# Kernel tuning notes

Measured on AMD Instinct MI355X. Metric: run time of the kernel, lower is better.

## Reference

```python
import jax, jax.numpy as jnp
import numpy as np
from jax import lax

B, DIM, H, W = 8, 256, 48, 48
HEADS, DH = 8, 32
K, S = 5, 2
P = K // 2
SCALE = DH ** -0.5
EPS = 1e-5


def setup_inputs() -> dict:
    key = jax.random.key(0)
    ks = jax.random.split(key, 12)
    w = lambda k, sh: jax.random.normal(k, sh, jnp.float32) * 0.02
    return {
        'x': jax.random.normal(ks[0], (B, DIM, H, W), jnp.float32),
        'kv': jax.random.normal(ks[1], (B, DIM, H, W), jnp.float32),
        'wq': w(ks[2], (DIM, DIM)), 'bq': jnp.zeros((DIM,), jnp.float32),
        'wk': w(ks[3], (DIM, DIM)), 'bk': jnp.zeros((DIM,), jnp.float32),
        'wv': w(ks[4], (DIM, DIM)), 'bv': jnp.zeros((DIM,), jnp.float32),
        'w_dw': w(ks[5], (DH, 1, K, K)), 'b_dw': jnp.zeros((DH,), jnp.float32),
        'ln_w': jnp.ones((DH,), jnp.float32), 'ln_b': jnp.zeros((DH,), jnp.float32),
        'w_off': w(ks[6], (2, DH)),
        'wo': w(ks[7], (DIM, DIM)), 'bo': jnp.zeros((DIM,), jnp.float32),
    }


def conv1x1(x, w, b=None):
    # x: (B, Cin, H, W), w: (Cout, Cin)
    y = jnp.einsum('oc,bchw->bohw', w, x)
    return y if b is None else y + b[None, :, None, None]


def grid_sample_bilinear(inp, grid):
    # inp: (N, C, Hh, Ww); grid: (N, Hg, Wg, 2) in (x, y), align_corners=True
    N, C, Hh, Ww = inp.shape
    gx = (grid[..., 0] + 1.0) * 0.5 * (Ww - 1)
    gy = (grid[..., 1] + 1.0) * 0.5 * (Hh - 1)
    x0 = jnp.floor(gx)
    y0 = jnp.floor(gy)
    wx = gx - x0  # frac weights for x1/y1 corners
    wy = gy - y0
    x0i = jnp.clip(x0.astype(jnp.int32), 0, Ww - 1)
    x1i = jnp.clip(x0.astype(jnp.int32) + 1, 0, Ww - 1)
    y0i = jnp.clip(y0.astype(jnp.int32), 0, Hh - 1)
    y1i = jnp.clip(y0.astype(jnp.int32) + 1, 0, Hh - 1)
    flat = inp.reshape(N, C, Hh * Ww)
    n = grid.shape[1] * grid.shape[2]

    def gather(yi, xi):
        idx = (yi * Ww + xi).reshape(N, 1, n)
        return jnp.take_along_axis(flat, jnp.broadcast_to(idx, (N, C, n)), axis=2)

    w00 = ((1 - wx) * (1 - wy)).reshape(N, 1, n)
    w01 = (wx * (1 - wy)).reshape(N, 1, n)
    w10 = ((1 - wx) * wy).reshape(N, 1, n)
    w11 = (wx * wy).reshape(N, 1, n)
    return (w00 * gather(y0i, x0i) + w01 * gather(y0i, x1i)
            + w10 * gather(y1i, x0i) + w11 * gather(y1i, x1i))  # (N, C, n)


def reference(x, kv, wq, bq, wk, bk, wv, bv, w_dw, b_dw, ln_w, ln_b, w_off, wo, bo):
    q = conv1x1(x, wq, bq)                      # (B, DIM, H, W)
    q_off = q.reshape(B * HEADS, DH, H, W)      # per-head channels
    # depthwise offset conv
    t = lax.conv_general_dilated(q_off, w_dw, (S, S), [(P, P), (P, P)],
                                 feature_group_count=DH,
                                 dimension_numbers=('NCHW', 'OIHW', 'NCHW'))
    t = t + b_dw[None, :, None, None]
    Hk, Wk = t.shape[2], t.shape[3]
    n = Hk * Wk
    # LayerNormProxy: LN over channel dim
    t = t.transpose(0, 2, 3, 1)                 # (BH, Hk, Wk, DH)
    mu = t.mean(-1, keepdims=True)
    var = ((t - mu) ** 2).mean(-1, keepdims=True)
    t = (t - mu) / jnp.sqrt(var + EPS) * ln_w + ln_b
    t = jax.nn.gelu(t, approximate=False)
    offset = jnp.einsum('oc,bhwc->bhwo', w_off, t)  # (BH, Hk, Wk, 2) as (y, x)
    # reference points, normalized to [-1, 1]
    ref_y = (jnp.linspace(0.5, Hk - 0.5, Hk, dtype=jnp.float32) / (Hk - 1.0)) * 2.0 - 1.0
    ref_x = (jnp.linspace(0.5, Wk - 0.5, Wk, dtype=jnp.float32) / (Wk - 1.0)) * 2.0 - 1.0
    ref = jnp.stack(jnp.meshgrid(ref_y, ref_x, indexing='ij'), axis=-1)  # (Hk, Wk, 2)
    pos = jnp.clip(offset + ref[None], -1.0, 1.0)
    grid = pos[..., ::-1]                       # (x, y) order for sampling
    kvs = grid_sample_bilinear(kv.reshape(B * HEADS, DH, H, W), grid)  # (BH, DH, n)
    kv4 = kvs.reshape(B, DIM, 1, n)
    k = conv1x1(kv4, wk, bk).reshape(B * HEADS, DH, n)
    v = conv1x1(kv4, wv, bv).reshape(B * HEADS, DH, n)
    qf = q.reshape(B * HEADS, DH, H * W)
    attn = jax.nn.softmax(jnp.einsum('bcm,bcn->bmn', qf, k) * SCALE, axis=2)
    out = jnp.einsum('bmn,bcn->bcm', attn, v).reshape(B, DIM, H, W)
    return conv1x1(out, wo, bo)
```

## Files before the change

### kernel.cpp

```cpp
#include <hip/hip_runtime.h>
#include <hip/hip_bf16.h>
#include <cstddef>

#define BB 8
#define DIM 256
#define HH 48
#define WW 48
#define HW 2304
#define HEADS 8
#define DH 32
#define BH 64
#define HK 24
#define WK 24
#define NN 576
#define SCALE 0.17677669529663687f
#define EPSF 1e-5f

typedef __attribute__((ext_vector_type(8))) short short8;
typedef __attribute__((ext_vector_type(4))) float f32x4;

static __device__ inline short f2bf_s(float f) {
  __hip_bfloat16 h = __float2bfloat16(f);
  return *reinterpret_cast<short*>(&h);
}

template <typename T> __device__ inline T cvt_out(float v);
template <> __device__ inline float cvt_out<float>(float v) { return v; }
template <> __device__ inline __hip_bfloat16 cvt_out<__hip_bfloat16>(float v) {
  return __float2bfloat16(v);
}

static __device__ inline unsigned pkrnd(float a, float b) {
  unsigned ua = __builtin_bit_cast(unsigned, a) + 0x8000u;
  unsigned ub = __builtin_bit_cast(unsigned, b) + 0x8000u;
  return __builtin_amdgcn_perm(ub, ua, 0x07060302);
}

static __device__ inline void split8(const float* xf, short8& bh, short8& bl) {
  union { unsigned u[4]; short8 v; } H, L;
#pragma unroll
  for (int p = 0; p < 4; p++) {
    float x0 = xf[2 * p], x1 = xf[2 * p + 1];
    unsigned u0 = __builtin_bit_cast(unsigned, x0) & 0xffff0000u;
    unsigned u1 = __builtin_bit_cast(unsigned, x1) & 0xffff0000u;
    float l0 = x0 - __builtin_bit_cast(float, u0);
    float l1 = x1 - __builtin_bit_cast(float, u1);
    H.u[p] = __builtin_amdgcn_perm(u1, u0, 0x07060302);
    L.u[p] = __builtin_amdgcn_perm(__builtin_bit_cast(unsigned, l1),
                                   __builtin_bit_cast(unsigned, l0), 0x07060302);
  }
  bh = H.v;
  bl = L.v;
}

__global__ __launch_bounds__(256) void split4(
    const float* __restrict__ w0, const float* __restrict__ w1,
    const float* __restrict__ w2, const float* __restrict__ w3,
    short* __restrict__ h0, short* __restrict__ l0,
    short* __restrict__ h1, short* __restrict__ l1,
    short* __restrict__ h2, short* __restrict__ l2,
    short* __restrict__ h3, short* __restrict__ l3) {
  const float* srcs[4] = {w0, w1, w2, w3};
  short* his[4] = {h0, h1, h2, h3};
  short* los[4] = {l0, l1, l2, l3};
  int sel = blockIdx.x >> 8;
  int i = (blockIdx.x & 255) * 256 + threadIdx.x;
  float v = srcs[sel][i];
  unsigned u = __builtin_bit_cast(unsigned, v) & 0xffff0000u;
  float rem = v - __builtin_bit_cast(float, u);
  his[sel][i] = (short)(u >> 16);
  los[sel][i] = (short)(__builtin_bit_cast(unsigned, rem) >> 16);
}

template <typename OT>
__global__ __launch_bounds__(64) void gemm_axf_mfma(const short* __restrict__ Wh,
                                                    const short* __restrict__ Wl,
                                                    const float* __restrict__ bias,
                                                    const float* __restrict__ X,
                                                    OT* __restrict__ Y, int M) {
  const int lane = threadIdx.x;
  const int quad = lane >> 4, l15 = lane & 15;
  const int b = blockIdx.z;
  const int oBase = blockIdx.y * 32;
  const int mBase = blockIdx.x * 64;
  const float* Xq = X + ((size_t)b * 256 + quad * 8) * M;

  f32x4 acc[2][4] = {};
  for (int kc = 0; kc < 256; kc += 32) {
    short8 ah0 = *(const short8*)(Wh + (size_t)(oBase + l15) * 256 + kc + quad * 8);
    short8 al0 = *(const short8*)(Wl + (size_t)(oBase + l15) * 256 + kc + quad * 8);
    short8 ah1 = *(const short8*)(Wh + (size_t)(oBase + 16 + l15) * 256 + kc + quad * 8);
    short8 al1 = *(const short8*)(Wl + (size_t)(oBase + 16 + l15) * 256 + kc + quad * 8);
#pragma unroll
    for (int mt = 0; mt < 4; mt++) {
      float xf[8];
      const float* xp = Xq + (size_t)kc * M + mBase + mt * 16 + l15;
#pragma unroll
      for (int j = 0; j < 8; j++) xf[j] = xp[(size_t)j * M];
      short8 bh, bl;
      split8(xf, bh, bl);
      acc[0][mt] = __builtin_amdgcn_mfma_f32_16x16x32_bf16(ah0, bh, acc[0][mt], 0, 0, 0);
      acc[0][mt] = __builtin_amdgcn_mfma_f32_16x16x32_bf16(al0, bh, acc[0][mt], 0, 0, 0);
      acc[0][mt] = __builtin_amdgcn_mfma_f32_16x16x32_bf16(ah0, bl, acc[0][mt], 0, 0, 0);
      acc[1][mt] = __builtin_amdgcn_mfma_f32_16x16x32_bf16(ah1, bh, acc[1][mt], 0, 0, 0);
      acc[1][mt] = __builtin_amdgcn_mfma_f32_16x16x32_bf16(al1, bh, acc[1][mt], 0, 0, 0);
      acc[1][mt] = __builtin_amdgcn_mfma_f32_16x16x32_bf16(ah1, bl, acc[1][mt], 0, 0, 0);
    }
  }

#pragma unroll
  for (int os = 0; os < 2; os++)
#pragma unroll
    for (int r = 0; r < 4; r++) {
      int o = oBase + os * 16 + quad * 4 + r;
      float bs = bias[o];
      OT* yp = Y + ((size_t)b * 256 + o) * M + mBase + l15;
#pragma unroll
      for (int mt = 0; mt < 4; mt++) yp[mt * 16] = cvt_out<OT>(acc[os][mt][r] + bs);
    }
}

__global__ __launch_bounds__(64) void k_gemm_mfma(const short* __restrict__ Wh,
                                                  const short* __restrict__ Wl,
                                                  const float* __restrict__ bias,
                                                  const float* __restrict__ X,
                                                  short* __restrict__ Y) {
  const int lane = threadIdx.x;
  const int quad = lane >> 4, l15 = lane & 15;
  const int b = blockIdx.z;
  const int nBase = blockIdx.x * 32;
  const int oBase = blockIdx.y * 64;
  const float* Xq = X + ((size_t)b * 256 + quad * 8) * NN;

  f32x4 acc[2][4] = {};
  for (int kc = 0; kc < 256; kc += 32) {
    short8 ah[2], al[2];
#pragma unroll
    for (int ns = 0; ns < 2; ns++) {
      float xf[8];
      const float* xp = Xq + (size_t)kc * NN + nBase + ns * 16 + l15;
#pragma unroll
      for (int j = 0; j < 8; j++) xf[j] = xp[(size_t)j * NN];
      split8(xf, ah[ns], al[ns]);
    }
#pragma unroll
    for (int ot = 0; ot < 4; ot++) {
      short8 bh = *(const short8*)(Wh + (size_t)(oBase + ot * 16 + l15) * 256 + kc + quad * 8);
      short8 bl = *(const short8*)(Wl + (size_t)(oBase + ot * 16 + l15) * 256 + kc + quad * 8);
#pragma unroll
      for (int ns = 0; ns < 2; ns++) {
        acc[ns][ot] = __builtin_amdgcn_mfma_f32_16x16x32_bf16(ah[ns], bh, acc[ns][ot], 0, 0, 0);
        acc[ns][ot] = __builtin_amdgcn_mfma_f32_16x16x32_bf16(al[ns], bh, acc[ns][ot], 0, 0, 0);
        acc[ns][ot] = __builtin_amdgcn_mfma_f32_16x16x32_bf16(ah[ns], bl, acc[ns][ot], 0, 0, 0);
      }
    }
  }

  float bs[4];
#pragma unroll
  for (int ot = 0; ot < 4; ot++) bs[ot] = bias[oBase + ot * 16 + l15];
#pragma unroll
  for (int ns = 0; ns < 2; ns++)
#pragma unroll
    for (int r = 0; r < 4; r++) {
      int n = nBase + ns * 16 + quad * 4 + r;
      short* yp = Y + ((size_t)b * NN + n) * 256 + oBase + l15;
#pragma unroll
      for (int ot = 0; ot < 4; ot++) yp[ot * 16] = f2bf_s(acc[ns][ot][r] + bs[ot]);
    }
}

__global__ __launch_bounds__(64) void dw_sample_kernel(
    const float* __restrict__ q, const float* __restrict__ kv,
    const float* __restrict__ w_dw, const float* __restrict__ b_dw,
    const float* __restrict__ ln_w, const float* __restrict__ ln_b,
    const float* __restrict__ w_off, float* __restrict__ kvs) {
  __shared__ float s_wdw[DH * 25];
  __shared__ float s_bdw[DH], s_lnw[DH], s_lnb[DH], s_woff[2 * DH];
  const int tid = threadIdx.x;
  for (int i = tid; i < DH * 25; i += 64) s_wdw[i] = w_dw[i];
  if (tid < DH) { s_bdw[tid] = b_dw[tid]; s_lnw[tid] = ln_w[tid]; s_lnb[tid] = ln_b[tid]; }
  if (tid < 2 * DH) s_woff[tid] = w_off[tid];
  __syncthreads();

  const int gid = blockIdx.x * 64 + tid;
  const int bh = gid / NN;
  const int n = gid - bh * NN;
  const int yk = n / WK, xk = n - yk * WK;

  const float* qb = q + (size_t)bh * DH * HW;
  float t[DH];
#pragma unroll
  for (int c = 0; c < DH; c++) t[c] = s_bdw[c];

  const int y0r = yk * 2 - 2, x0r = xk * 2 - 2;
  for (int dy = 0; dy < 5; dy++) {
    int y = y0r + dy;
    if (y < 0 || y >= HH) continue;
    for (int dx = 0; dx < 5; dx++) {
      int x = x0r + dx;
      if (x < 0 || x >= WW) continue;
      int off = y * WW + x;
      int widx = dy * 5 + dx;
#pragma unroll
      for (int c = 0; c < DH; c++)
        t[c] += s_wdw[c * 25 + widx] * qb[c * HW + off];
    }
  }

  float mu = 0.f;
#pragma unroll
  for (int c = 0; c < DH; c++) mu += t[c];
  mu *= (1.0f / DH);
  float var = 0.f;
#pragma unroll
  for (int c = 0; c < DH; c++) { float d = t[c] - mu; var += d * d; }
  var *= (1.0f / DH);
  float rstd = rsqrtf(var + EPSF);

  float o0 = 0.f, o1 = 0.f;
#pragma unroll
  for (int c = 0; c < DH; c++) {
    float xn = (t[c] - mu) * rstd * s_lnw[c] + s_lnb[c];
    float g = 0.5f * xn * (1.0f + erff(xn * 0.70710678118654752f));
    o0 += s_woff[c] * g;
    o1 += s_woff[DH + c] * g;
  }

  const float ref_y = (0.5f + (float)yk) / 23.0f * 2.0f - 1.0f;
  const float ref_x = (0.5f + (float)xk) / 23.0f * 2.0f - 1.0f;
  float py = fminf(fmaxf(o0 + ref_y, -1.0f), 1.0f);
  float px = fminf(fmaxf(o1 + ref_x, -1.0f), 1.0f);

  float gx = (px + 1.0f) * 0.5f * 47.0f;
  float gy = (py + 1.0f) * 0.5f * 47.0f;
  float x0f = floorf(gx), y0f = floorf(gy);
  float wx = gx - x0f, wy = gy - y0f;
  int x0 = (int)x0f, y0 = (int)y0f;
  int x0i = min(max(x0, 0), WW - 1);
  int x1i = min(max(x0 + 1, 0), WW - 1);
  int y0i = min(max(y0, 0), HH - 1);
  int y1i = min(max(y0 + 1, 0), HH - 1);
  float w00 = (1.f - wx) * (1.f - wy);
  float w01 = wx * (1.f - wy);
  float w10 = (1.f - wx) * wy;
  float w11 = wx * wy;
  int i00 = y0i * WW + x0i, i01 = y0i * WW + x1i;
  int i10 = y1i * WW + x0i, i11 = y1i * WW + x1i;

  const float* kvb = kv + (size_t)bh * DH * HW;
#pragma unroll
  for (int c = 0; c < DH; c++) {
    const float* p = kvb + (size_t)c * HW;
    float val = w00 * p[i00] + w01 * p[i01] + w10 * p[i10] + w11 * p[i11];
    kvs[((size_t)bh * DH + c) * NN + n] = val;
  }
}

__global__ __launch_bounds__(256) void attn_mfma(const float* __restrict__ q,
                                                 const short* __restrict__ Kb,
                                                 const short* __restrict__ Vb,
                                                 short* __restrict__ O) {
  __shared__ int smem[2][4][2][256];
  const int tid = threadIdx.x;
  const int wave = tid >> 6;
  const int lane = tid & 63;
  const int quad = lane >> 4;
  const int l15 = lane & 15;
  const int bh = blockIdx.y;
  const int b = bh >> 3, head = bh & 7;
  const int mBase = blockIdx.x * 128 + wave * 32;

  short8 bq[2];
#pragma unroll
  for (int mt = 0; mt < 2; mt++) {
    const float* qp = q + ((size_t)bh * DH + quad * 8) * HW + mBase + mt * 16 + l15;
    short8 v;
#pragma unroll
    for (int j = 0; j < 8; j++) v[j] = f2bf_s(qp[(size_t)j * HW] * SCALE);
    bq[mt] = v;
  }

  const short* kbase = Kb + (size_t)b * NN * 256 + head * DH + quad * 8;
  const short* vb0 = Vb + ((size_t)b * 256 + head * DH + l15) * NN + quad * 8;
  const short* vb1 = vb0 + (size_t)16 * NN;

  f32x4 oacc[2][2] = {};
  float dsum[2] = {0.f, 0.f};

  const int row16 = l15 * 16;
  const int wr0 = row16 + (((quad >> 1) ^ (l15 & 3)) << 2) + ((quad & 1) << 1);
  const int wr1 = row16 + (((2 + (quad >> 1)) ^ (l15 & 3)) << 2) + ((quad & 1) << 1);
  const int rd = row16 + ((quad ^ (l15 & 3)) << 2);

  short8 ka0 = *(const short8*)(kbase + (size_t)l15 * 256);
  short8 ka1 = *(const short8*)(kbase + (size_t)(16 + l15) * 256);

  for (int it = 0; it < NN / 32; it++) {
    const int nb = it * 32;
    short8 va0 = *(const short8*)(vb0 + nb);
    short8 va1 = *(const short8*)(vb1 + nb);
    f32x4 z = {0.f, 0.f, 0.f, 0.f};
    f32x4 st[2][2];
    st[0][0] = __builtin_amdgcn_mfma_f32_16x16x32_bf16(ka0, bq[0], z, 0, 0, 0);
    st[0][1] = __builtin_amdgcn_mfma_f32_16x16x32_bf16(ka1, bq[0], z, 0, 0, 0);
    st[1][0] = __builtin_amdgcn_mfma_f32_16x16x32_bf16(ka0, bq[1], z, 0, 0, 0);
    st[1][1] = __builtin_amdgcn_mfma_f32_16x16x32_bf16(ka1, bq[1], z, 0, 0, 0);
    if (it + 1 < NN / 32) {
      ka0 = *(const short8*)(kbase + (size_t)(nb + 32 + l15) * 256);
      ka1 = *(const short8*)(kbase + (size_t)(nb + 48 + l15) * 256);
    }
    int* sm = &smem[it & 1][wave][0][0];
#pragma unroll
    for (int mt = 0; mt < 2; mt++) {
      float p0 = __expf(st[mt][0][0]), p1 = __expf(st[mt][0][1]);
      float p2 = __expf(st[mt][0][2]), p3 = __expf(st[mt][0][3]);
      float p4 = __expf(st[mt][1][0]), p5 = __expf(st[mt][1][1]);
      float p6 = __expf(st[mt][1][2]), p7 = __expf(st[mt][1][3]);
      dsum[mt] += ((p0 + p1) + (p2 + p3)) + ((p4 + p5) + (p6 + p7));
      int* base = sm + mt * 256;
      *(int2*)(base + wr0) = make_int2((int)pkrnd(p0, p1), (int)pkrnd(p2, p3));
      *(int2*)(base + wr1) = make_int2((int)pkrnd(p4, p5), (int)pkrnd(p6, p7));
    }
#pragma unroll
    for (int mt = 0; mt < 2; mt++) {
      short8 pa = *(short8*)(sm + mt * 256 + rd);
      oacc[mt][0] = __builtin_amdgcn_mfma_f32_16x16x32_bf16(pa, va0, oacc[mt][0], 0, 0, 0);
      oacc[mt][1] = __builtin_amdgcn_mfma_f32_16x16x32_bf16(pa, va1, oacc[mt][1], 0, 0, 0);
    }
  }

#pragma unroll
  for (int mt = 0; mt < 2; mt++) {
    float d = dsum[mt];
    d += __shfl_xor(d, 16);
    d += __shfl_xor(d, 32);
    short* ob = O + ((size_t)b * HW + mBase + mt * 16) * 256 + head * DH + l15;
#pragma unroll
    for (int r = 0; r < 4; r++) {
      float dr = __shfl(d, quad * 4 + r);
      float inv = 1.0f / dr;
      ob[(size_t)(quad * 4 + r) * 256] = f2bf_s(oacc[mt][0][r] * inv);
      ob[(size_t)(quad * 4 + r) * 256 + 16] = f2bf_s(oacc[mt][1][r] * inv);
    }
  }
}

__global__ __launch_bounds__(256) void wo_gemm_mfma(const short* __restrict__ Whi,
                                                    const short* __restrict__ Wlo,
                                                    const float* __restrict__ bias,
                                                    const short* __restrict__ X,
                                                    float* __restrict__ Y) {
  const int tid = threadIdx.x;
  const int wave = tid >> 6;
  const int lane = tid & 63;
  const int quad = lane >> 4;
  const int l15 = lane & 15;
  const int b = blockIdx.z;
  const int oBase = blockIdx.y * 64 + wave * 16;
  const int mBase = blockIdx.x * 64;

  const short* wh = Whi + (size_t)(oBase + l15) * 256 + quad * 8;
  const short* wl = Wlo + (size_t)(oBase + l15) * 256 + quad * 8;
  const short* xb = X + ((size_t)b * HW + mBase) * 256 + quad * 8;

  f32x4 acc[4] = {};

  for (int k = 0; k < 256; k += 32) {
    short8 ah = *(const short8*)(wh + k);
    short8 al = *(const short8*)(wl + k);
#pragma unroll
    for (int mt = 0; mt < 4; mt++) {
      short8 bx = *(const short8*)(xb + (size_t)(mt * 16 + l15) * 256 + k);
      acc[mt] = __builtin_amdgcn_mfma_f32_16x16x32_bf16(ah, bx, acc[mt], 0, 0, 0);
      acc[mt] = __builtin_amdgcn_mfma_f32_16x16x32_bf16(al, bx, acc[mt], 0, 0, 0);
    }
  }

#pragma unroll
  for (int r = 0; r < 4; r++) {
    int o = oBase + quad * 4 + r;
    float bs = bias[o];
    float* yrow = Y + ((size_t)b * 256 + o) * HW + mBase + l15;
#pragma unroll
    for (int mt = 0; mt < 4; mt++) {
      yrow[mt * 16] = acc[mt][r] + bs;
    }
  }
}

extern "C" void kernel_launch(void* const* d_in, const int* in_sizes, int n_in,
                              void* d_out, int out_size, void* d_ws, size_t ws_size,
                              hipStream_t stream) {
  const float* x    = (const float*)d_in[0];
  const float* kv   = (const float*)d_in[1];
  const float* wq   = (const float*)d_in[2];
  const float* bq   = (const float*)d_in[3];
  const float* wk   = (const float*)d_in[4];
  const float* bk   = (const float*)d_in[5];
  const float* wv   = (const float*)d_in[6];
  const float* bv   = (const float*)d_in[7];
  const float* w_dw = (const float*)d_in[8];
  const float* b_dw = (const float*)d_in[9];
  const float* ln_w = (const float*)d_in[10];
  const float* ln_b = (const float*)d_in[11];
  const float* w_off= (const float*)d_in[12];
  const float* wo   = (const float*)d_in[13];
  const float* bo   = (const float*)d_in[14];
  float* out = (float*)d_out;
  float* ws = (float*)d_ws;

  float* q   = ws;
  float* kvs = ws + 4718592;
  short* O   = (short*)(ws + 4718592);
  short* Kb  = (short*)(ws + 7077888);
  short* Vb  = (short*)(ws + 7667712);
  short* Wqh = (short*)(ws + 8257536);
  short* Wql = Wqh + 65536;
  short* Wkh = Wql + 65536;
  short* Wkl = Wkh + 65536;
  short* Wvh = Wkl + 65536;
  short* Wvl = Wvh + 65536;
  short* Woh = Wvl + 65536;
  short* Wol = Woh + 65536;

  split4<<<dim3(1024), dim3(256), 0, stream>>>(wq, wk, wv, wo, Wqh, Wql, Wkh, Wkl,
                                               Wvh, Wvl, Woh, Wol);
  gemm_axf_mfma<float><<<dim3(HW / 64, 8, BB), dim3(64), 0, stream>>>(
      Wqh, Wql, bq, x, q, HW);
  dw_sample_kernel<<<dim3(BH * NN / 64), dim3(64), 0, stream>>>(
      q, kv, w_dw, b_dw, ln_w, ln_b, w_off, kvs);
  k_gemm_mfma<<<dim3(NN / 32, 4, BB), dim3(64), 0, stream>>>(Wkh, Wkl, bk, kvs, Kb);
  gemm_axf_mfma<__hip_bfloat16><<<dim3(NN / 64, 8, BB), dim3(64), 0, stream>>>(
      Wvh, Wvl, bv, kvs, (__hip_bfloat16*)Vb, NN);
  attn_mfma<<<dim3(HW / 128, BH), dim3(256), 0, stream>>>(q, Kb, Vb, O);
  wo_gemm_mfma<<<dim3(HW / 64, 4, BB), dim3(256), 0, stream>>>(Woh, Wol, bo, O, out);
}
```

Measured before the change: 270.8 us.

## Retile Q projection, split dw_sample channels across lanes, shrink attention per-wave tile

Adds a dedicated Q-projection GEMM kernel in which each 256-thread block computes all 256 output channels for a 64-pixel tile, so every X load is reused across four output slices. The depthwise/offset/sample kernel now spreads the 32 channels of one sample across four lane groups of 8, using shuffles for the LayerNorm and offset reductions, which gives 4x more threads and smaller register arrays. The attention kernel processes 16 query rows per wave instead of 32, doubling the grid to raise parallelism, at the cost of reloading K/V per wave more often. The LDS swizzle pattern is also changed.

```diff
diff --git a/kernel.cpp b/kernel.cpp
--- a/kernel.cpp
+++ b/kernel.cpp
@@ -72,6 +72,57 @@
   los[sel][i] = (short)(__builtin_bit_cast(unsigned, rem) >> 16);
 }
 
+__global__ __launch_bounds__(256) void gemm_q_mfma(const short* __restrict__ Wh,
+                                                   const short* __restrict__ Wl,
+                                                   const float* __restrict__ bias,
+                                                   const float* __restrict__ X,
+                                                   float* __restrict__ Y) {
+  const int tid = threadIdx.x;
+  const int wave = tid >> 6;
+  const int lane = tid & 63;
+  const int quad = lane >> 4, l15 = lane & 15;
+  const int b = blockIdx.y;
+  const int oBase = wave * 64;
+  const int mBase = blockIdx.x * 64;
+  const float* Xq = X + ((size_t)b * 256 + quad * 8) * HW;
+
+  f32x4 acc[4][4] = {};
+  for (int kc = 0; kc < 256; kc += 32) {
+    short8 ah[4], al[4];
+#pragma unroll
+    for (int os = 0; os < 4; os++) {
+      ah[os] = *(const short8*)(Wh + (size_t)(oBase + os * 16 + l15) * 256 + kc + quad * 8);
+      al[os] = *(const short8*)(Wl + (size_t)(oBase + os * 16 + l15) * 256 + kc + quad * 8);
+    }
+#pragma unroll
+    for (int mt = 0; mt < 4; mt++) {
+      float xf[8];
+      const float* xp = Xq + (size_t)kc * HW + mBase + mt * 16 + l15;
+#pragma unroll
+      for (int j = 0; j < 8; j++) xf[j] = xp[(size_t)j * HW];
+      short8 bh, bl;
+      split8(xf, bh, bl);
+#pragma unroll
+      for (int os = 0; os < 4; os++) {
+        acc[os][mt] = __builtin_amdgcn_mfma_f32_16x16x32_bf16(ah[os], bh, acc[os][mt], 0, 0, 0);
+        acc[os][mt] = __builtin_amdgcn_mfma_f32_16x16x32_bf16(al[os], bh, acc[os][mt], 0, 0, 0);
+        acc[os][mt] = __builtin_amdgcn_mfma_f32_16x16x32_bf16(ah[os], bl, acc[os][mt], 0, 0, 0);
+      }
+    }
+  }
+
+#pragma unroll
+  for (int os = 0; os < 4; os++)
+#pragma unroll
+    for (int r = 0; r < 4; r++) {
+      int o = oBase + os * 16 + quad * 4 + r;
+      float bs = bias[o];
+      float* yp = Y + ((size_t)b * 256 + o) * HW + mBase + l15;
+#pragma unroll
+      for (int mt = 0; mt < 4; mt++) yp[mt * 16] = acc[os][mt][r] + bs;
+    }
+}
+
 template <typename OT>
 __global__ __launch_bounds__(64) void gemm_axf_mfma(const short* __restrict__ Wh,
                                                     const short* __restrict__ Wl,
@@ -183,15 +234,17 @@
   if (tid < 2 * DH) s_woff[tid] = w_off[tid];
   __syncthreads();
 
-  const int gid = blockIdx.x * 64 + tid;
-  const int bh = gid / NN;
-  const int n = gid - bh * NN;
+  const int nl = tid & 15, cg = tid >> 4;
+  const int c0 = cg * 8;
+  const int bh = blockIdx.x / (NN / 16);
+  const int ntile = blockIdx.x - bh * (NN / 16);
+  const int n = ntile * 16 + nl;
   const int yk = n / WK, xk = n - yk * WK;
 
   const float* qb = q + (size_t)bh * DH * HW;
-  float t[DH];
-#pragma unroll
-  for (int c = 0; c < DH; c++) t[c] = s_bdw[c];
+  float t[8];
+#pragma unroll
+  for (int j = 0; j < 8; j++) t[j] = s_bdw[c0 + j];
 
   const int y0r = yk * 2 - 2, x0r = xk * 2 - 2;
   for (int dy = 0; dy < 5; dy++) {
@@ -203,29 +256,37 @@
       int off = y * WW + x;
       int widx = dy * 5 + dx;
 #pragma unroll
-      for (int c = 0; c < DH; c++)
-        t[c] += s_wdw[c * 25 + widx] * qb[c * HW + off];
+      for (int j = 0; j < 8; j++)
+        t[j] += s_wdw[(c0 + j) * 25 + widx] * qb[(size_t)(c0 + j) * HW + off];
     }
   }
 
   float mu = 0.f;
 #pragma unroll
-  for (int c = 0; c < DH; c++) mu += t[c];
+  for (int j = 0; j < 8; j++) mu += t[j];
+  mu += __shfl_xor(mu, 16);
+  mu += __shfl_xor(mu, 32);
   mu *= (1.0f / DH);
   float var = 0.f;
 #pragma unroll
-  for (int c = 0; c < DH; c++) { float d = t[c] - mu; var += d * d; }
+  for (int j = 0; j < 8; j++) { float d = t[j] - mu; var += d * d; }
+  var += __shfl_xor(var, 16);
+  var += __shfl_xor(var, 32);
   var *= (1.0f / DH);
   float rstd = rsqrtf(var + EPSF);
 
   float o0 = 0.f, o1 = 0.f;
 #pragma unroll
-  for (int c = 0; c < DH; c++) {
-    float xn = (t[c] - mu) * rstd * s_lnw[c] + s_lnb[c];
+  for (int j = 0; j < 8; j++) {
+    float xn = (t[j] - mu) * rstd * s_lnw[c0 + j] + s_lnb[c0 + j];
     float g = 0.5f * xn * (1.0f + erff(xn * 0.70710678118654752f));
-    o0 += s_woff[c] * g;
-    o1 += s_woff[DH + c] * g;
-  }
+    o0 += s_woff[c0 + j] * g;
+    o1 += s_woff[DH + c0 + j] * g;
+  }
+  o0 += __shfl_xor(o0, 16);
+  o0 += __shfl_xor(o0, 32);
+  o1 += __shfl_xor(o1, 16);
+  o1 += __shfl_xor(o1, 32);
 
   const float ref_y = (0.5f + (float)yk) / 23.0f * 2.0f - 1.0f;
   const float ref_x = (0.5f + (float)xk) / 23.0f * 2.0f - 1.0f;
@@ -248,12 +309,12 @@
   int i00 = y0i * WW + x0i, i01 = y0i * WW + x1i;
   int i10 = y1i * WW + x0i, i11 = y1i * WW + x1i;
 
-  const float* kvb = kv + (size_t)bh * DH * HW;
-#pragma unroll
-  for (int c = 0; c < DH; c++) {
-    const float* p = kvb + (size_t)c * HW;
+  const float* kvb = kv + ((size_t)bh * DH + c0) * HW;
+#pragma unroll
+  for (int j = 0; j < 8; j++) {
+    const float* p = kvb + (size_t)j * HW;
     float val = w00 * p[i00] + w01 * p[i01] + w10 * p[i10] + w11 * p[i11];
-    kvs[((size_t)bh * DH + c) * NN + n] = val;
+    kvs[((size_t)bh * DH + c0 + j) * NN + n] = val;
   }
 }
 
@@ -261,7 +322,7 @@
                                                  const short* __restrict__ Kb,
                                                  const short* __restrict__ Vb,
                                                  short* __restrict__ O) {
-  __shared__ int smem[2][4][2][256];
+  __shared__ int smem[2][4][256];
   const int tid = threadIdx.x;
   const int wave = tid >> 6;
   const int lane = tid & 63;
@@ -269,29 +330,27 @@
   const int l15 = lane & 15;
   const int bh = blockIdx.y;
   const int b = bh >> 3, head = bh & 7;
-  const int mBase = blockIdx.x * 128 + wave * 32;
-
-  short8 bq[2];
-#pragma unroll
-  for (int mt = 0; mt < 2; mt++) {
-    const float* qp = q + ((size_t)bh * DH + quad * 8) * HW + mBase + mt * 16 + l15;
-    short8 v;
-#pragma unroll
-    for (int j = 0; j < 8; j++) v[j] = f2bf_s(qp[(size_t)j * HW] * SCALE);
-    bq[mt] = v;
+  const int mBase = blockIdx.x * 64 + wave * 16;
+
+  short8 bq;
+  {
+    const float* qp = q + ((size_t)bh * DH + quad * 8) * HW + mBase + l15;
+#pragma unroll
+    for (int j = 0; j < 8; j++) bq[j] = f2bf_s(qp[(size_t)j * HW] * SCALE);
   }
 
   const short* kbase = Kb + (size_t)b * NN * 256 + head * DH + quad * 8;
   const short* vb0 = Vb + ((size_t)b * 256 + head * DH + l15) * NN + quad * 8;
   const short* vb1 = vb0 + (size_t)16 * NN;
 
-  f32x4 oacc[2][2] = {};
-  float dsum[2] = {0.f, 0.f};
-
+  f32x4 oacc0 = {}, oacc1 = {};
+  float dsum = 0.f;
+
+  const int g = (l15 >> 1) & 3;
   const int row16 = l15 * 16;
-  const int wr0 = row16 + (((quad >> 1) ^ (l15 & 3)) << 2) + ((quad & 1) << 1);
-  const int wr1 = row16 + (((2 + (quad >> 1)) ^ (l15 & 3)) << 2) + ((quad & 1) << 1);
-  const int rd = row16 + ((quad ^ (l15 & 3)) << 2);
+  const int wr0 = row16 + ((((quad >> 1)) ^ g) << 2) + ((quad & 1) << 1);
+  const int wr1 = row16 + (((2 + (quad >> 1)) ^ g) << 2) + ((quad & 1) << 1);
+  const int rd = row16 + ((quad ^ g) << 2);
 
   short8 ka0 = *(const short8*)(kbase + (size_t)l15 * 256);
   short8 ka1 = *(const short8*)(kbase + (size_t)(16 + l15) * 256);
@@ -301,48 +360,36 @@
     short8 va0 = *(const short8*)(vb0 + nb);
     short8 va1 = *(const short8*)(vb1 + nb);
     f32x4 z = {0.f, 0.f, 0.f, 0.f};
-    f32x4 st[2][2];
-    st[0][0] = __builtin_amdgcn_mfma_f32_16x16x32_bf16(ka0, bq[0], z, 0, 0, 0);
-    st[0][1] = __builtin_amdgcn_mfma_f32_16x16x32_bf16(ka1, bq[0], z, 0, 0, 0);
-    st[1][0] = __builtin_amdgcn_mfma_f32_16x16x32_bf16(ka0, bq[1], z, 0, 0, 0);
-    st[1][1] = __builtin_amdgcn_mfma_f32_16x16x32_bf16(ka1, bq[1], z, 0, 0, 0);
+    f32x4 st0 = __builtin_amdgcn_mfma_f32_16x16x32_bf16(ka0, bq, z, 0, 0, 0);
+    f32x4 st1 = __builtin_amdgcn_mfma_f32_16x16x32_bf16(ka1, bq, z, 0, 0, 0);
     if (it + 1 < NN / 32) {
       ka0 = *(const short8*)(kbase + (size_t)(nb + 32 + l15) * 256);
       ka1 = *(const short8*)(kbase + (size_t)(nb + 48 + l15) * 256);
     }
-    int* sm = &smem[it & 1][wave][0][0];
-#pragma unroll
-    for (int mt = 0; mt < 2; mt++) {
-      float p0 = __expf(st[mt][0][0]), p1 = __expf(st[mt][0][1]);
-      float p2 = __expf(st[mt][0][2]), p3 = __expf(st[mt][0][3]);
-      float p4 = __expf(st[mt][1][0]), p5 = __expf(st[mt][1][1]);
-      float p6 = __expf(st[mt][1][2]), p7 = __expf(st[mt][1][3]);
-      dsum[mt] += ((p0 + p1) + (p2 + p3)) + ((p4 + p5) + (p6 + p7));
-      int* base = sm + mt * 256;
-      *(int2*)(base + wr0) = make_int2((int)pkrnd(p0, p1), (int)pkrnd(p2, p3));
-      *(int2*)(base + wr1) = make_int2((int)pkrnd(p4, p5), (int)pkrnd(p6, p7));
-    }
-#pragma unroll
-    for (int mt = 0; mt < 2; mt++) {
-      short8 pa = *(short8*)(sm + mt * 256 + rd);
-      oacc[mt][0] = __builtin_amdgcn_mfma_f32_16x16x32_bf16(pa, va0, oacc[mt][0], 0, 0, 0);
-      oacc[mt][1] = __builtin_amdgcn_mfma_f32_16x16x32_bf16(pa, va1, oacc[mt][1], 0, 0, 0);
-    }
-  }
-
-#pragma unroll
-  for (int mt = 0; mt < 2; mt++) {
-    float d = dsum[mt];
-    d += __shfl_xor(d, 16);
-    d += __shfl_xor(d, 32);
-    short* ob = O + ((size_t)b * HW + mBase + mt * 16) * 256 + head * DH + l15;
-#pragma unroll
-    for (int r = 0; r < 4; r++) {
-      float dr = __shfl(d, quad * 4 + r);
-      float inv = 1.0f / dr;
-      ob[(size_t)(quad * 4 + r) * 256] = f2bf_s(oacc[mt][0][r] * inv);
-      ob[(size_t)(quad * 4 + r) * 256 + 16] = f2bf_s(oacc[mt][1][r] * inv);
-    }
+    float p0 = __expf(st0[0]), p1 = __expf(st0[1]);
+    float p2 = __expf(st0[2]), p3 = __expf(st0[3]);
+    float p4 = __expf(st1[0]), p5 = __expf(st1[1]);
+    float p6 = __expf(st1[2]), p7 = __expf(st1[3]);
+    dsum += ((p0 + p1) + (p2 + p3)) + ((p4 + p5) + (p6 + p7));
+    int* sm = &smem[it & 1][wave][0];
+    *(int2*)(sm + wr0) = make_int2((int)pkrnd(p0, p1), (int)pkrnd(p2, p3));
+    *(int2*)(sm + wr1) = make_int2((int)pkrnd(p4, p5), (int)pkrnd(p6, p7));
+    short8 pa = *(short8*)(sm + rd);
+    oacc0 = __builtin_amdgcn_mfma_f32_16x16x32_bf16(pa, va0, oacc0, 0, 0, 0);
+    oacc1 = __builtin_amdgcn_mfma_f32_16x16x32_bf16(pa, va1, oacc1, 0, 0, 0);
+  }
+
+  float d = dsum;
+  d += __shfl_xor(d, 16);
+  d += __shfl_xor(d, 32);
+
+  short* ob = O + ((size_t)b * HW + mBase) * 256 + head * DH + l15;
+#pragma unroll
+  for (int r = 0; r < 4; r++) {
+    float dr = __shfl(d, quad * 4 + r);
+    float inv = 1.0f / dr;
+    ob[(size_t)(quad * 4 + r) * 256] = f2bf_s(oacc0[r] * inv);
+    ob[(size_t)(quad * 4 + r) * 256 + 16] = f2bf_s(oacc1[r] * inv);
   }
 }
 
@@ -426,13 +473,12 @@
 
   split4<<<dim3(1024), dim3(256), 0, stream>>>(wq, wk, wv, wo, Wqh, Wql, Wkh, Wkl,
                                                Wvh, Wvl, Woh, Wol);
-  gemm_axf_mfma<float><<<dim3(HW / 64, 8, BB), dim3(64), 0, stream>>>(
-      Wqh, Wql, bq, x, q, HW);
-  dw_sample_kernel<<<dim3(BH * NN / 64), dim3(64), 0, stream>>>(
+  gemm_q_mfma<<<dim3(HW / 64, BB), dim3(256), 0, stream>>>(Wqh, Wql, bq, x, q);
+  dw_sample_kernel<<<dim3(BH * NN / 16), dim3(64), 0, stream>>>(
       q, kv, w_dw, b_dw, ln_w, ln_b, w_off, kvs);
   k_gemm_mfma<<<dim3(NN / 32, 4, BB), dim3(64), 0, stream>>>(Wkh, Wkl, bk, kvs, Kb);
   gemm_axf_mfma<__hip_bfloat16><<<dim3(NN / 64, 8, BB), dim3(64), 0, stream>>>(
       Wvh, Wvl, bv, kvs, (__hip_bfloat16*)Vb, NN);
-  attn_mfma<<<dim3(HW / 128, BH), dim3(256), 0, stream>>>(q, Kb, Vb, O);
+  attn_mfma<<<dim3(HW / 64, BH), dim3(256), 0, stream>>>(q, Kb, Vb, O);
   wo_gemm_mfma<<<dim3(HW / 64, 4, BB), dim3(256), 0, stream>>>(Woh, Wol, bo, O, out);
 }
```

Measured after the change: 298.8 us. 10.3% more time.
